# Performance work log

Hardware: AMD Instinct MI355X
Metric: run time of the kernel (lower is better)

## Reference

```python
import jax, jax.numpy as jnp
import numpy as np

B, S, D, H, DH = 2, 2048, 2048, 16, 128
ROT_DIM = 128
ROT_BASE = 10000.0
ATTN_SCALE = float(np.sqrt(DH))


def _sin_cos_rotary(n_ctx, rotary_dim, base):
    pos = jnp.arange(n_ctx, dtype=jnp.float32)
    dim = jnp.arange(rotary_dim // 2, dtype=jnp.float32)
    freq = base ** (dim / (rotary_dim / 2))
    freq = jnp.concatenate([freq, freq])  # non-adjacent pairs: '(2 d)' layout
    angles = pos[:, None] / freq[None, :]  # [n_ctx, rotary_dim]
    return jnp.sin(angles), jnp.cos(angles)


def _rotate_every_two(x):
    # non-adjacent-pairs rotation: [-x2, x1] on halves of last dim
    d = x.shape[-1]
    return jnp.concatenate([-x[..., d // 2:], x[..., :d // 2]], axis=-1)


def _apply_rotary(x, sin, cos):
    # x: [batch, pos, head, d_head]
    n = x.shape[1]
    x_rot = x[..., :ROT_DIM]
    x_pass = x[..., ROT_DIM:]
    c = cos[:n][None, :, None, :]
    s = sin[:n][None, :, None, :]
    x_rotated = x_rot * c + _rotate_every_two(x_rot) * s
    return jnp.concatenate([x_rotated, x_pass], axis=-1)


def setup_inputs() -> dict:
    key = jax.random.key(0)
    ks = jax.random.split(key, 8)
    init = 0.02
    return {
        'query_input': jax.random.normal(ks[0], (B, S, D), jnp.float32),
        'key_input': jax.random.normal(ks[1], (B, S, D), jnp.float32),
        'value_input': jax.random.normal(ks[2], (B, S, D), jnp.float32),
        'W_Q': jax.random.normal(ks[3], (H, D, DH), jnp.float32) * init,
        'W_K': jax.random.normal(ks[4], (H, D, DH), jnp.float32) * init,
        'W_V': jax.random.normal(ks[5], (H, D, DH), jnp.float32) * init,
        'W_O': jax.random.normal(ks[6], (H, DH, D), jnp.float32) * init,
        'b_Q': jnp.zeros((H, DH), jnp.float32),
        'b_K': jnp.zeros((H, DH), jnp.float32),
        'b_V': jnp.zeros((H, DH), jnp.float32),
        'b_O': jnp.zeros((D,), jnp.float32),
    }


def reference(query_input, key_input, value_input, W_Q, W_K, W_V, W_O, b_Q, b_K, b_V, b_O):
    # QKV projections: [b, pos, d_model] x [h, d_model, d_head] -> [b, pos, h, d_head]
    q = jnp.einsum('bpd,hde->bphe', query_input, W_Q) + b_Q
    k = jnp.einsum('bpd,hde->bphe', key_input, W_K) + b_K
    v = jnp.einsum('bpd,hde->bphe', value_input, W_V) + b_V

    sin, cos = _sin_cos_rotary(S, ROT_DIM, ROT_BASE)
    q = _apply_rotary(q, sin, cos)
    k = _apply_rotary(k, sin, cos)

    # attention scores [b, h, q_pos, k_pos]
    scores = jnp.einsum('bqhe,bkhe->bhqk', q, k) / ATTN_SCALE
    causal = jnp.tril(jnp.ones((S, S), bool))
    scores = jnp.where(causal[None, None], scores, -jnp.inf)
    pattern = jax.nn.softmax(scores, axis=-1)
    pattern = jnp.where(jnp.isnan(pattern), jnp.zeros_like(pattern), pattern)

    z = jnp.einsum('bhqk,bkhe->bqhe', pattern, v)
    out = jnp.einsum('bqhe,hed->bqd', z, W_O) + b_O
    return out
```

## Files before the change

kernel.cpp:

```cpp
#include <hip/hip_runtime.h>
#include <hip/hip_bf16.h>
#include <cmath>

typedef __bf16 bf16;
typedef __bf16 bf16x8 __attribute__((ext_vector_type(8)));
typedef __bf16 bf16x4 __attribute__((ext_vector_type(4)));
typedef float  f32x4  __attribute__((ext_vector_type(4)));


__global__ void xcvt_kernel(const float* __restrict__ a, const float* __restrict__ b,
                            const float* __restrict__ c,
                            bf16* __restrict__ oa, bf16* __restrict__ ob, bf16* __restrict__ oc) {
    int i = (blockIdx.x * 256 + threadIdx.x) * 4;
    float4 va = *(const float4*)(a + i);
    float4 vb = *(const float4*)(b + i);
    float4 vc = *(const float4*)(c + i);
    bf16x4 ra = { (bf16)va.x, (bf16)va.y, (bf16)va.z, (bf16)va.w };
    bf16x4 rb = { (bf16)vb.x, (bf16)vb.y, (bf16)vb.z, (bf16)vb.w };
    bf16x4 rc = { (bf16)vc.x, (bf16)vc.y, (bf16)vc.z, (bf16)vc.w };
    *(bf16x4*)(oa + i) = ra;
    *(bf16x4*)(ob + i) = rb;
    *(bf16x4*)(oc + i) = rc;
}

// ... 15 lines not shown
        dst = (z == 0) ? WQT : (z == 1) ? WKT : WVT;
        int h = bx >> 6, rem = bx & 63;
        int d0 = (rem >> 1) << 6, e0 = (rem & 1) << 6;
        sbase = (long)h * 262144 + (long)d0 * 128 + e0;
        sRS = 128;
        dbase = (long)(h * 128 + e0) * 2048 + d0;
    } else {
        src = WO; dst = WOT;
        int a0 = (bx >> 5) << 6, b0 = (bx & 31) << 6;
        sbase = (long)a0 * 2048 + b0;
        sRS = 2048;
        dbase = (long)b0 * 2048 + a0;
    }

#pragma unroll
    for (int p = 0; p < 4; p++) {
        int r = p * 16 + tr;
        float4 v = *(const float4*)(src + sbase + (long)r * sRS + tc);
        T[r * 65 + tc]     = v.x;
        T[r * 65 + tc + 1] = v.y;
        T[r * 65 + tc + 2] = v.z;
        T[r * 65 + tc + 3] = v.w;
    }
    __syncthreads();
#pragma unroll
    for (int p = 0; p < 4; p++) {
        int rr = p * 16 + tr;
        bf16x4 o = { (bf16)T[tc * 65 + rr],       (bf16)T[(tc + 1) * 65 + rr],
                     (bf16)T[(tc + 2) * 65 + rr], (bf16)T[(tc + 3) * 65 + rr] };
        *(bf16x4*)(dst + dbase + (long)rr * 2048 + tc) = o;
    }
}

__launch_bounds__(256)
__global__ void qkv_gemm_kernel(const bf16* __restrict__ XQ, const bf16* __restrict__ XK,
                                const bf16* __restrict__ XV,
                                const bf16* __restrict__ WQT, const bf16* __restrict__ WKT,
                                const bf16* __restrict__ WVT,
                                const float* __restrict__ bQ, const float* __restrict__ bK,
                                const float* __restrict__ bV,
                                bf16* __restrict__ QB, bf16* __restrict__ KB,
                                bf16* __restrict__ VT) {
    __shared__ __align__(16) bf16 As[128 * 32];
    __shared__ __align__(16) bf16 Bs[128 * 32];
    __shared__ __align__(16) bf16 Cs[64 * 136];
    const int z = blockIdx.z;
    const bf16* A  = (z == 0) ? XQ  : (z == 1) ? XK  : XV;
    const bf16* Bm = (z == 0) ? WQT : (z == 1) ? WKT : WVT;
    const float* bias = (z == 0) ? bQ : (z == 1) ? bK : bV;

    const int tid = threadIdx.x;
    const int w = tid >> 6, lane = tid & 63;
    const int quad = lane >> 4, l16 = lane & 15;
    const int wm = w & 1, wn = w >> 1;
    const int m_base = blockIdx.x << 7, n_base = blockIdx.y << 7;

    const int srow = lane >> 2;
    const int scol = (lane & 3) << 3;
    const int ab0 = w * 2, ab1 = w * 2 + 1;
    const bf16* gA0 = A  + (long)(m_base + ab0 * 16 + srow) * 2048 + scol;
    const bf16* gA1 = A  + (long)(m_base + ab1 * 16 + srow) * 2048 + scol;
    const bf16* gB0 = Bm + (long)(n_base + ab0 * 16 + srow) * 2048 + scol;
    const bf16* gB1 = Bm + (long)(n_base + ab1 * 16 + srow) * 2048 + scol;
    bf16* lA0 = &As[ab0 * 512];
    bf16* lA1 = &As[ab1 * 512];
    bf16* lB0 = &Bs[ab0 * 512];
    bf16* lB1 = &Bs[ab1 * 512];

    f32x4 acc[4][4] = {};

    for (int k0 = 0; k0 < 2048; k0 += 32) {
        __builtin_amdgcn_global_load_lds((const __attribute__((address_space(1))) void*)(gA0 + k0),
                                         (__attribute__((address_space(3))) void*)lA0, 16, 0, 0);
        __builtin_amdgcn_global_load_lds((const __attribute__((address_space(1))) void*)(gA1 + k0),
                                         (__attribute__((address_space(3))) void*)lA1, 16, 0, 0);
        __builtin_amdgcn_global_load_lds((const __attribute__((address_space(1))) void*)(gB0 + k0),
                                         (__attribute__((address_space(3))) void*)lB0, 16, 0, 0);
        __builtin_amdgcn_global_load_lds((const __attribute__((address_space(1))) void*)(gB1 + k0),
                                         (__attribute__((address_space(3))) void*)lB1, 16, 0, 0);
        __syncthreads();

        bf16x8 af[4], bfr[4];
#pragma unroll
        for (int mt = 0; mt < 4; mt++)
            af[mt] = *(const bf16x8*)&As[((wm * 64 + mt * 16 + l16) << 5) + (quad << 3)];
#pragma unroll
        for (int nt = 0; nt < 4; nt++) {
            int nrow = wn * 32 + (nt & 1) * 16 + (nt >> 1) * 64 + l16;
            bfr[nt] = *(const bf16x8*)&Bs[(nrow << 5) + (quad << 3)];
        }
#pragma unroll
        for (int mt = 0; mt < 4; mt++)
#pragma unroll
            for (int nt = 0; nt < 4; nt++)
                acc[mt][nt] = __builtin_amdgcn_mfma_f32_16x16x32_bf16(af[mt], bfr[nt], acc[mt][nt], 0, 0, 0);
        __syncthreads();
    }

    const int bq = m_base >> 11;
    const int h  = n_base >> 7;
    const long obase = ((long)(bq * 16 + h)) << 18;

    if (z <= 1) {
        bf16* O = (z == 0) ? QB : KB;
        const float scl = (z == 0) ? 0.08838834764831845f : 1.0f;
#pragma unroll
        for (int nt = 0; nt < 2; nt++) {
            const int e_lo = wn * 32 + nt * 16 + l16;
            const float bv_lo = bias[n_base + e_lo];
            const float bv_hi = bias[n_base + e_lo + 64];
            const float inv_freq = exp2f((float)e_lo * -0.20762050593046f);
#pragma unroll
            for (int mt = 0; mt < 4; mt++) {
#pragma unroll
                for (int r = 0; r < 4; r++) {
                    int s = (m_base & 2047) + wm * 64 + mt * 16 + quad * 4 + r;
                    float sn, cs;
                    __sincosf((float)s * inv_freq, &sn, &cs);
                    float x0 = acc[mt][nt][r]     + bv_lo;
                    float x1 = acc[mt][nt + 2][r] + bv_hi;
                    O[obase + ((long)s << 7) + e_lo]      = (bf16)((x0 * cs - x1 * sn) * scl);
                    O[obase + ((long)s << 7) + e_lo + 64] = (bf16)((x1 * cs + x0 * sn) * scl);
                }
            }
        }
    } else {
#pragma unroll
        for (int eh = 0; eh < 2; eh++) {
#pragma unroll
            for (int nt2 = 0; nt2 < 2; nt2++) {
                const int nt = eh * 2 + nt2;
                const int e_l = wn * 32 + nt2 * 16 + l16;
                const float bv = bias[n_base + eh * 64 + e_l];
#pragma unroll
                for (int mt = 0; mt < 4; mt++) {
                    int s0 = wm * 64 + mt * 16 + quad * 4;
                    bf16x4 pk = { (bf16)(acc[mt][nt][0] + bv), (bf16)(acc[mt][nt][1] + bv),
                                  (bf16)(acc[mt][nt][2] + bv), (bf16)(acc[mt][nt][3] + bv) };
                    *(bf16x4*)&Cs[e_l * 136 + s0] = pk;
                }
            }
            __syncthreads();
            {
                const int e_l = tid >> 2;
                const int sq  = (tid & 3) << 5;
                const int e   = eh * 64 + e_l;
                const long vb = obase + ((long)e << 11) + (m_base & 2047) + sq;
#pragma unroll
                for (int j = 0; j < 4; j++)
                    *(bf16x8*)&VT[vb + j * 8] = *(const bf16x8*)&Cs[e_l * 136 + sq + j * 8];
            }
            __syncthreads();
        }
    }
}

__launch_bounds__(256, 3)
__global__ void flash_kernel(const bf16* __restrict__ Q, const bf16* __restrict__ K,
                             const bf16* __restrict__ Vt, bf16* __restrict__ Z) {
    __shared__ __align__(16) bf16 Ks[64 * 136];
    __shared__ __align__(16) bf16 Vs[128 * 72];
    __shared__ __align__(16) bf16 Ps[64 * 72];
    const int tid = threadIdx.x, w = tid >> 6, lane = tid & 63;
    const int quad = lane >> 4, l16 = lane & 15;
    const int n = blockIdx.x;
    const int bh = (n & 7) | (((n >> 3) & 3) << 3);
    const int qt = 31 - (n >> 5);
    const int b = bh >> 4, h = bh & 15;
    const long qk_base = (long)bh << 18;
    const int qbase = qt << 6;
    const float FM = 12.0f;

    const int kr_row = tid >> 4;
    const int kr_col = (tid & 15) << 3;
    const int vr_row = tid >> 3;
    const int vr_col = (tid & 7) << 3;
    const bf16* Kg = K  + qk_base + (long)kr_row * 128 + kr_col;
    const bf16* Vg = Vt + qk_base + (long)vr_row * 2048 + vr_col;

    bf16x8 qf[4];
#pragma unroll
    for (int ks = 0; ks < 4; ks++)
        qf[ks] = *(const bf16x8*)(Q + qk_base + ((long)(qbase + w * 16 + l16) << 7) + ks * 32 + (quad << 3));

    bf16x8 va[4], ka[4], vb2[4], kb[4];
#pragma unroll
    for (int p = 0; p < 4; p++) va[p] = *(const bf16x8*)(Vg + (long)p * 65536);
// ... 48 lines not shown
                Ps[(w * 16 + quad * 4 + r) * 72 + nt * 16 + l16] = (bf16)p;
            }

#pragma unroll
        for (int kk = 0; kk < 2; kk++) {
            bf16x8 pf = *(const bf16x8*)&Ps[(w * 16 + l16) * 72 + kk * 32 + (quad << 3)];
#pragma unroll
            for (int dt = 0; dt < 8; dt++) {
                bf16x8 vf = *(const bf16x8*)&Vs[(dt * 16 + l16) * 72 + kk * 32 + (quad << 3)];
                o[dt] = __builtin_amdgcn_mfma_f32_16x16x32_bf16(pf, vf, o[dt], 0, 0, 0);
            }
        }
        __syncthreads();

#pragma unroll
        for (int p = 0; p < 4; p++) va[p] = vb2[p];
#pragma unroll
        for (int p = 0; p < 4; p++) ka[p] = kb[p];
    }

#pragma unroll
    for (int r = 0; r < 4; r++) {
        float l = lsum[r];
        l += __shfl_xor(l, 1);
        l += __shfl_xor(l, 2);
        l += __shfl_xor(l, 4);
        l += __shfl_xor(l, 8);
        float inv = 1.f / l;
        int qrow = qbase + w * 16 + quad * 4 + r;
        long zr = ((long)(b * 2048 + qrow) << 11) + h * 128;
#pragma unroll
        for (int dt = 0; dt < 8; dt++)
            Z[zr + dt * 16 + l16] = (bf16)(o[dt][r] * inv);
    }
}

__launch_bounds__(256)
__global__ void gemm_o_kernel(const bf16* __restrict__ A, const bf16* __restrict__ Bm,
                              const float* __restrict__ bias, float* __restrict__ Of) {
    __shared__ __align__(16) bf16 As[128 * 32];
    __shared__ __align__(16) bf16 Bs[128 * 32];
    const int tid = threadIdx.x;
    const int w = tid >> 6, lane = tid & 63;
    const int quad = lane >> 4, l16 = lane & 15;
    const int wm = w & 1, wn = w >> 1;
    const int m_base = blockIdx.x << 7, n_base = blockIdx.y << 7;

    const int srow = lane >> 2;
    const int scol = (lane & 3) << 3;
    const int ab0 = w * 2, ab1 = w * 2 + 1;
    const bf16* gA0 = A  + (long)(m_base + ab0 * 16 + srow) * 2048 + scol;
    const bf16* gA1 = A  + (long)(m_base + ab1 * 16 + srow) * 2048 + scol;
    const bf16* gB0 = Bm + (long)(n_base + ab0 * 16 + srow) * 2048 + scol;
    const bf16* gB1 = Bm + (long)(n_base + ab1 * 16 + srow) * 2048 + scol;
    bf16* lA0 = &As[ab0 * 512];
    bf16* lA1 = &As[ab1 * 512];
    bf16* lB0 = &Bs[ab0 * 512];
    bf16* lB1 = &Bs[ab1 * 512];

    f32x4 acc[4][4] = {};

    for (int k0 = 0; k0 < 2048; k0 += 32) {
        __builtin_amdgcn_global_load_lds((const __attribute__((address_space(1))) void*)(gA0 + k0),
                                         (__attribute__((address_space(3))) void*)lA0, 16, 0, 0);
        __builtin_amdgcn_global_load_lds((const __attribute__((address_space(1))) void*)(gA1 + k0),
                                         (__attribute__((address_space(3))) void*)lA1, 16, 0, 0);
        __builtin_amdgcn_global_load_lds((const __attribute__((address_space(1))) void*)(gB0 + k0),
                                         (__attribute__((address_space(3))) void*)lB0, 16, 0, 0);
        __builtin_amdgcn_global_load_lds((const __attribute__((address_space(1))) void*)(gB1 + k0),
                                         (__attribute__((address_space(3))) void*)lB1, 16, 0, 0);
        __syncthreads();

        bf16x8 af[4], bfr[4];
#pragma unroll
        for (int mt = 0; mt < 4; mt++)
            af[mt] = *(const bf16x8*)&As[((wm * 64 + mt * 16 + l16) << 5) + (quad << 3)];
#pragma unroll
        for (int nt = 0; nt < 4; nt++)
            bfr[nt] = *(const bf16x8*)&Bs[((wn * 64 + nt * 16 + l16) << 5) + (quad << 3)];
#pragma unroll
        for (int mt = 0; mt < 4; mt++)
#pragma unroll
            for (int nt = 0; nt < 4; nt++)
                acc[mt][nt] = __builtin_amdgcn_mfma_f32_16x16x32_bf16(af[mt], bfr[nt], acc[mt][nt], 0, 0, 0);
        __syncthreads();
    }

#pragma unroll
    for (int nt = 0; nt < 4; nt++) {
        int col = n_base + wn * 64 + nt * 16 + l16;
        float bv = bias[col];
#pragma unroll
        for (int mt = 0; mt < 4; mt++) {
#pragma unroll
            for (int r = 0; r < 4; r++) {
                int row = m_base + wm * 64 + mt * 16 + quad * 4 + r;
                Of[((long)row << 11) + col] = acc[mt][nt][r] + bv;
            }
        }
    }
}

extern "C" void kernel_launch(void* const* d_in, const int* in_sizes, int n_in,
                              void* d_out, int out_size, void* d_ws, size_t ws_size,
                              hipStream_t stream) {
    (void)in_sizes; (void)n_in; (void)out_size; (void)ws_size;
    const float* qin = (const float*)d_in[0];
    const float* kin = (const float*)d_in[1];
    const float* vin = (const float*)d_in[2];
    const float* WQ  = (const float*)d_in[3];
    const float* WK  = (const float*)d_in[4];
    const float* WV  = (const float*)d_in[5];
    const float* WO  = (const float*)d_in[6];
    const float* bQ  = (const float*)d_in[7];
    const float* bK  = (const float*)d_in[8];
    const float* bV  = (const float*)d_in[9];
    const float* bO  = (const float*)d_in[10];
    float* out = (float*)d_out;

    bf16* ws = (bf16*)d_ws;
    bf16* XQ  = ws + 0L;
    bf16* XK  = ws + 8388608L;
    bf16* XV  = ws + 16777216L;
    bf16* WQT = ws + 25165824L;
    bf16* WKT = ws + 29360128L;
    bf16* WVT = ws + 33554432L;
    bf16* WOT = ws + 37748736L;
    bf16* QB  = ws + 41943040L;
    bf16* KB  = ws + 50331648L;
    bf16* VT  = ws + 58720256L;
    bf16* Z   = XQ;

    xcvt_kernel<<<8192, 256, 0, stream>>>(qin, kin, vin, XQ, XK, XV);
    wtr_kernel<<<dim3(1024, 4), 256, 0, stream>>>(WQ, WK, WV, WO, WQT, WKT, WVT, WOT);
    qkv_gemm_kernel<<<dim3(32, 16, 3), 256, 0, stream>>>(XQ, XK, XV, WQT, WKT, WVT,
                                                         bQ, bK, bV, QB, KB, VT);
    flash_kernel<<<1024, 256, 0, stream>>>(QB, KB, VT, Z);
    gemm_o_kernel<<<dim3(32, 16), 256, 0, stream>>>(Z, WOT, bO, out);
}
```

Baseline: 426.4 us.

## Rewrite QKV GEMM as 256x256 tile with 8 waves and double-buffered swizzled LDS

The QKV projection GEMM moves from 128x128 tiles with 4 waves to 256x256 tiles with 8 waves (512 threads) and a K-step of 64. Operand tiles are double-buffered in 128 KB of LDS with an XOR swizzle, and global-to-LDS loads for the next stages are interleaved between four MFMA phases using barriers and s_setprio. The goal is more data reuse per byte loaded, fewer LDS bank conflicts, and overlap of memory traffic with matrix math. In exchange the grid shrinks to 384 blocks, occupancy is limited by the large LDS footprint, and the epilogue is reworked to fit the new tile mapping.

```diff
diff --git a/kernel.cpp b/kernel.cpp
--- a/kernel.cpp
+++ b/kernel.cpp
@@ -71,7 +71,7 @@
     }
 }
 
-__launch_bounds__(256)
+__launch_bounds__(512, 2)
 __global__ void qkv_gemm_kernel(const bf16* __restrict__ XQ, const bf16* __restrict__ XK,
                                 const bf16* __restrict__ XV,
                                 const bf16* __restrict__ WQT, const bf16* __restrict__ WKT,
@@ -80,9 +80,7 @@
                                 const float* __restrict__ bV,
                                 bf16* __restrict__ QB, bf16* __restrict__ KB,
                                 bf16* __restrict__ VT) {
-    __shared__ __align__(16) bf16 As[128 * 32];
-    __shared__ __align__(16) bf16 Bs[128 * 32];
-    __shared__ __align__(16) bf16 Cs[64 * 136];
+    __shared__ __align__(1024) char SMb[131072];
     const int z = blockIdx.z;
     const bf16* A  = (z == 0) ? XQ  : (z == 1) ? XK  : XV;
     const bf16* Bm = (z == 0) ? WQT : (z == 1) ? WKT : WVT;
@@ -92,104 +90,178 @@
     const int w = tid >> 6, lane = tid & 63;
     const int quad = lane >> 4, l16 = lane & 15;
     const int wm = w & 1, wn = w >> 1;
-    const int m_base = blockIdx.x << 7, n_base = blockIdx.y << 7;
-
-    const int srow = lane >> 2;
-    const int scol = (lane & 3) << 3;
-    const int ab0 = w * 2, ab1 = w * 2 + 1;
-    const bf16* gA0 = A  + (long)(m_base + ab0 * 16 + srow) * 2048 + scol;
-    const bf16* gA1 = A  + (long)(m_base + ab1 * 16 + srow) * 2048 + scol;
-    const bf16* gB0 = Bm + (long)(n_base + ab0 * 16 + srow) * 2048 + scol;
-    const bf16* gB1 = Bm + (long)(n_base + ab1 * 16 + srow) * 2048 + scol;
-    bf16* lA0 = &As[ab0 * 512];
-    bf16* lA1 = &As[ab1 * 512];
-    bf16* lB0 = &Bs[ab0 * 512];
-    bf16* lB1 = &Bs[ab1 * 512];
-
-    f32x4 acc[4][4] = {};
-
-    for (int k0 = 0; k0 < 2048; k0 += 32) {
-        __builtin_amdgcn_global_load_lds((const __attribute__((address_space(1))) void*)(gA0 + k0),
-                                         (__attribute__((address_space(3))) void*)lA0, 16, 0, 0);
-        __builtin_amdgcn_global_load_lds((const __attribute__((address_space(1))) void*)(gA1 + k0),
-                                         (__attribute__((address_space(3))) void*)lA1, 16, 0, 0);
-        __builtin_amdgcn_global_load_lds((const __attribute__((address_space(1))) void*)(gB0 + k0),
-                                         (__attribute__((address_space(3))) void*)lB0, 16, 0, 0);
-        __builtin_amdgcn_global_load_lds((const __attribute__((address_space(1))) void*)(gB1 + k0),
-                                         (__attribute__((address_space(3))) void*)lB1, 16, 0, 0);
-        __syncthreads();
-
-        bf16x8 af[4], bfr[4];
-#pragma unroll
-        for (int mt = 0; mt < 4; mt++)
-            af[mt] = *(const bf16x8*)&As[((wm * 64 + mt * 16 + l16) << 5) + (quad << 3)];
-#pragma unroll
-        for (int nt = 0; nt < 4; nt++) {
-            int nrow = wn * 32 + (nt & 1) * 16 + (nt >> 1) * 64 + l16;
-            bfr[nt] = *(const bf16x8*)&Bs[(nrow << 5) + (quad << 3)];
-        }
-#pragma unroll
-        for (int mt = 0; mt < 4; mt++)
-#pragma unroll
-            for (int nt = 0; nt < 4; nt++)
-                acc[mt][nt] = __builtin_amdgcn_mfma_f32_16x16x32_bf16(af[mt], bfr[nt], acc[mt][nt], 0, 0, 0);
-        __syncthreads();
-    }
-
-    const int bq = m_base >> 11;
-    const int h  = n_base >> 7;
-    const long obase = ((long)(bq * 16 + h)) << 18;
+    const int m_base = blockIdx.x << 8, n_base = blockIdx.y << 8;
+
+    const int lr = lane >> 3;
+    const int lc = ((lane & 7) ^ lr) << 3;
+    const bf16* gA = A  + (long)(m_base + (w << 4) + lr) * 2048 + lc;
+    const bf16* gB = Bm + (long)(n_base + (w << 4) + lr) * 2048 + lc;
+    char* dstBase = SMb + (w << 11);
+
+#define STAGE(T, opB, half) do {                                                              \
+    const bf16* _s = ((opB) ? gB : gA) + (long)((half) * 128) * 2048 + (T) * 64;              \
+    char* _d = dstBase + (((T) & 1) * 65536 + (opB) * 32768 + (half) * 16384);                \
+    __builtin_amdgcn_global_load_lds((const __attribute__((address_space(1))) void*)_s,       \
+        (__attribute__((address_space(3))) void*)_d, 16, 0, 0);                               \
+    __builtin_amdgcn_global_load_lds((const __attribute__((address_space(1))) void*)(_s + 16384), \
+        (__attribute__((address_space(3))) void*)(_d + 1024), 16, 0, 0);                      \
+} while (0)
+
+    f32x4 acc[8][4] = {};
+    bf16x8 af[4][2], bg[4][2];
+    const int cb0 = quad << 4;
+
+    STAGE(0, 1, 0); STAGE(0, 1, 1); STAGE(0, 0, 0); STAGE(0, 0, 1);
+    STAGE(1, 1, 0); STAGE(1, 1, 1);
+    asm volatile("s_waitcnt vmcnt(4)" ::: "memory");
+    __builtin_amdgcn_s_barrier();
+
+    for (int t = 0; t < 32; ++t) {
+        const int bufA = (t & 1) * 65536 + wm * 16384;
+        const int bufB = (t & 1) * 65536 + 32768 + (wn >> 1) * 16384;
+
+#pragma unroll
+        for (int mt = 0; mt < 4; mt++) {
+            int r = mt * 16 + l16, sw = (r & 7) << 4;
+            af[mt][0] = *(const bf16x8*)(SMb + bufA + r * 128 + (cb0 ^ sw));
+            af[mt][1] = *(const bf16x8*)(SMb + bufA + r * 128 + ((64 + cb0) ^ sw));
+        }
+#pragma unroll
+        for (int nt = 0; nt < 2; nt++) {
+            int r = nt * 64 + (wn & 1) * 32 + l16, sw = (r & 7) << 4;
+            bg[nt][0] = *(const bf16x8*)(SMb + bufB + r * 128 + (cb0 ^ sw));
+            bg[nt][1] = *(const bf16x8*)(SMb + bufB + r * 128 + ((64 + cb0) ^ sw));
+        }
+        if (t < 31) STAGE(t + 1, 0, 0);
+        __builtin_amdgcn_s_barrier();
+        __builtin_amdgcn_s_setprio(1);
+#pragma unroll
+        for (int mt = 0; mt < 4; mt++)
+#pragma unroll
+            for (int nt = 0; nt < 2; nt++) {
+                acc[mt][nt] = __builtin_amdgcn_mfma_f32_16x16x32_bf16(af[mt][0], bg[nt][0], acc[mt][nt], 0, 0, 0);
+                acc[mt][nt] = __builtin_amdgcn_mfma_f32_16x16x32_bf16(af[mt][1], bg[nt][1], acc[mt][nt], 0, 0, 0);
+            }
+        __builtin_amdgcn_s_setprio(0);
+        __builtin_amdgcn_s_barrier();
+
+#pragma unroll
+        for (int nt = 2; nt < 4; nt++) {
+            int r = (nt & 1) * 64 + (wn & 1) * 32 + 16 + l16, sw = (r & 7) << 4;
+            bg[nt][0] = *(const bf16x8*)(SMb + bufB + r * 128 + (cb0 ^ sw));
+            bg[nt][1] = *(const bf16x8*)(SMb + bufB + r * 128 + ((64 + cb0) ^ sw));
+        }
+        if (t < 31) STAGE(t + 1, 0, 1);
+        __builtin_amdgcn_s_barrier();
+        __builtin_amdgcn_s_setprio(1);
+#pragma unroll
+        for (int mt = 0; mt < 4; mt++)
+#pragma unroll
+            for (int nt = 2; nt < 4; nt++) {
+                acc[mt][nt] = __builtin_amdgcn_mfma_f32_16x16x32_bf16(af[mt][0], bg[nt][0], acc[mt][nt], 0, 0, 0);
+                acc[mt][nt] = __builtin_amdgcn_mfma_f32_16x16x32_bf16(af[mt][1], bg[nt][1], acc[mt][nt], 0, 0, 0);
+            }
+        __builtin_amdgcn_s_setprio(0);
+        __builtin_amdgcn_s_barrier();
+
+#pragma unroll
+        for (int mt = 0; mt < 4; mt++) {
+            int r = 64 + mt * 16 + l16, sw = (r & 7) << 4;
+            af[mt][0] = *(const bf16x8*)(SMb + bufA + r * 128 + (cb0 ^ sw));
+            af[mt][1] = *(const bf16x8*)(SMb + bufA + r * 128 + ((64 + cb0) ^ sw));
+        }
+        if (t < 30) STAGE(t + 2, 1, 0);
+        __builtin_amdgcn_s_barrier();
+        __builtin_amdgcn_s_setprio(1);
+#pragma unroll
+        for (int mt = 0; mt < 4; mt++)
+#pragma unroll
+            for (int nt = 2; nt < 4; nt++) {
+                acc[4 + mt][nt] = __builtin_amdgcn_mfma_f32_16x16x32_bf16(af[mt][0], bg[nt][0], acc[4 + mt][nt], 0, 0, 0);
+                acc[4 + mt][nt] = __builtin_amdgcn_mfma_f32_16x16x32_bf16(af[mt][1], bg[nt][1], acc[4 + mt][nt], 0, 0, 0);
+            }
+        __builtin_amdgcn_s_setprio(0);
+        __builtin_amdgcn_s_barrier();
+
+        if (t < 30) STAGE(t + 2, 1, 1);
+        __builtin_amdgcn_s_barrier();
+        __builtin_amdgcn_s_setprio(1);
+#pragma unroll
+        for (int mt = 0; mt < 4; mt++)
+#pragma unroll
+            for (int nt = 0; nt < 2; nt++) {
+                acc[4 + mt][nt] = __builtin_amdgcn_mfma_f32_16x16x32_bf16(af[mt][0], bg[nt][0], acc[4 + mt][nt], 0, 0, 0);
+                acc[4 + mt][nt] = __builtin_amdgcn_mfma_f32_16x16x32_bf16(af[mt][1], bg[nt][1], acc[4 + mt][nt], 0, 0, 0);
+            }
+        __builtin_amdgcn_s_setprio(0);
+        if (t == 30) { asm volatile("s_waitcnt vmcnt(0)" ::: "memory"); }
+        else         { asm volatile("s_waitcnt vmcnt(4)" ::: "memory"); }
+        __builtin_amdgcn_s_barrier();
+    }
+#undef STAGE
+
+    const int bq = blockIdx.x >> 3;
+    const int by = blockIdx.y;
 
     if (z <= 1) {
         bf16* O = (z == 0) ? QB : KB;
         const float scl = (z == 0) ? 0.08838834764831845f : 1.0f;
-#pragma unroll
-        for (int nt = 0; nt < 2; nt++) {
-            const int e_lo = wn * 32 + nt * 16 + l16;
-            const float bv_lo = bias[n_base + e_lo];
-            const float bv_hi = bias[n_base + e_lo + 64];
+        const int h = by * 2 + (wn >> 1);
+        const long obase = ((long)(bq * 16 + h)) << 18;
+#pragma unroll
+        for (int p = 0; p < 2; p++) {
+            const int e_lo = (wn & 1) * 32 + p * 16 + l16;
+            const float bv_lo = bias[n_base + (wn >> 1) * 128 + e_lo];
+            const float bv_hi = bias[n_base + (wn >> 1) * 128 + e_lo + 64];
             const float inv_freq = exp2f((float)e_lo * -0.20762050593046f);
-#pragma unroll
-            for (int mt = 0; mt < 4; mt++) {
+            const int ntL = p * 2, ntH = p * 2 + 1;
+#pragma unroll
+            for (int mt = 0; mt < 8; mt++) {
 #pragma unroll
                 for (int r = 0; r < 4; r++) {
-                    int s = (m_base & 2047) + wm * 64 + mt * 16 + quad * 4 + r;
+                    int s = (m_base & 2047) + wm * 128 + mt * 16 + quad * 4 + r;
                     float sn, cs;
                     __sincosf((float)s * inv_freq, &sn, &cs);
-                    float x0 = acc[mt][nt][r]     + bv_lo;
-                    float x1 = acc[mt][nt + 2][r] + bv_hi;
+                    float x0 = acc[mt][ntL][r] + bv_lo;
+                    float x1 = acc[mt][ntH][r] + bv_hi;
                     O[obase + ((long)s << 7) + e_lo]      = (bf16)((x0 * cs - x1 * sn) * scl);
                     O[obase + ((long)s << 7) + e_lo + 64] = (bf16)((x1 * cs + x0 * sn) * scl);
                 }
             }
         }
     } else {
+        bf16* Ct = (bf16*)SMb;
 #pragma unroll
         for (int eh = 0; eh < 2; eh++) {
-#pragma unroll
-            for (int nt2 = 0; nt2 < 2; nt2++) {
-                const int nt = eh * 2 + nt2;
-                const int e_l = wn * 32 + nt2 * 16 + l16;
-                const float bv = bias[n_base + eh * 64 + e_l];
-#pragma unroll
-                for (int mt = 0; mt < 4; mt++) {
-                    int s0 = wm * 64 + mt * 16 + quad * 4;
-                    bf16x4 pk = { (bf16)(acc[mt][nt][0] + bv), (bf16)(acc[mt][nt][1] + bv),
-                                  (bf16)(acc[mt][nt][2] + bv), (bf16)(acc[mt][nt][3] + bv) };
-                    *(bf16x4*)&Cs[e_l * 136 + s0] = pk;
-                }
+            __syncthreads();
+            if ((wn >> 1) == eh) {
+#pragma unroll
+                for (int p = 0; p < 2; p++)
+#pragma unroll
+                    for (int hi = 0; hi < 2; hi++) {
+                        const int nt = p * 2 + hi;
+                        const int e_l = (wn & 1) * 32 + p * 16 + l16 + hi * 64;
+                        const float bv = bias[n_base + eh * 128 + e_l];
+#pragma unroll
+                        for (int mt = 0; mt < 8; mt++) {
+                            int s0 = wm * 128 + mt * 16 + quad * 4;
+                            bf16x4 pk = { (bf16)(acc[mt][nt][0] + bv), (bf16)(acc[mt][nt][1] + bv),
+                                          (bf16)(acc[mt][nt][2] + bv), (bf16)(acc[mt][nt][3] + bv) };
+                            *(bf16x4*)&Ct[e_l * 264 + s0] = pk;
+                        }
+                    }
             }
             __syncthreads();
             {
                 const int e_l = tid >> 2;
-                const int sq  = (tid & 3) << 5;
-                const int e   = eh * 64 + e_l;
-                const long vb = obase + ((long)e << 11) + (m_base & 2047) + sq;
-#pragma unroll
-                for (int j = 0; j < 4; j++)
-                    *(bf16x8*)&VT[vb + j * 8] = *(const bf16x8*)&Cs[e_l * 136 + sq + j * 8];
-            }
-            __syncthreads();
+                const int sq  = (tid & 3) << 6;
+                const int hgl = by * 2 + eh;
+                const long vb = (((long)(bq * 16 + hgl)) << 18) + ((long)e_l << 11)
+                              + (m_base & 2047) + sq;
+#pragma unroll
+                for (int j = 0; j < 8; j++)
+                    *(bf16x8*)&VT[vb + j * 8] = *(const bf16x8*)&Ct[e_l * 264 + sq + j * 8];
+            }
         }
     }
 }
@@ -407,8 +479,8 @@
 
     xcvt_kernel<<<8192, 256, 0, stream>>>(qin, kin, vin, XQ, XK, XV);
     wtr_kernel<<<dim3(1024, 4), 256, 0, stream>>>(WQ, WK, WV, WO, WQT, WKT, WVT, WOT);
-    qkv_gemm_kernel<<<dim3(32, 16, 3), 256, 0, stream>>>(XQ, XK, XV, WQT, WKT, WVT,
-                                                         bQ, bK, bV, QB, KB, VT);
+    qkv_gemm_kernel<<<dim3(16, 8, 3), 512, 0, stream>>>(XQ, XK, XV, WQT, WKT, WVT,
+                                                        bQ, bK, bV, QB, KB, VT);
     flash_kernel<<<1024, 256, 0, stream>>>(QB, KB, VT, Z);
     gemm_o_kernel<<<dim3(32, 16), 256, 0, stream>>>(Z, WOT, bO, out);
 }
```

After: 437.8 us. +2.7%, slower.

## Rewrite QKV GEMM with 256x128 tiles, 512 threads, double-buffered swizzled LDS

Applied to the files above, without the earlier changes.

The QKV projection GEMM now uses 512-thread blocks computing 256x128 tiles with BK=64. Global-to-LDS loads are double-buffered across iterations and overlapped with MFMA work using explicit waitcnt, barriers and setprio. An XOR swizzle on the LDS layout avoids bank conflicts. The aim is to hide load latency and raise MFMA utilisation, at the cost of 96KB of LDS per block, which limits occupancy, and of fewer blocks in the grid.

```diff
diff --git a/kernel.cpp b/kernel.cpp
--- a/kernel.cpp
+++ b/kernel.cpp
@@ -71,7 +71,7 @@
     }
 }
 
-__launch_bounds__(256)
+__launch_bounds__(512, 2)
 __global__ void qkv_gemm_kernel(const bf16* __restrict__ XQ, const bf16* __restrict__ XK,
                                 const bf16* __restrict__ XV,
                                 const bf16* __restrict__ WQT, const bf16* __restrict__ WKT,
@@ -80,9 +80,7 @@
                                 const float* __restrict__ bV,
                                 bf16* __restrict__ QB, bf16* __restrict__ KB,
                                 bf16* __restrict__ VT) {
-    __shared__ __align__(16) bf16 As[128 * 32];
-    __shared__ __align__(16) bf16 Bs[128 * 32];
-    __shared__ __align__(16) bf16 Cs[64 * 136];
+    __shared__ __align__(1024) char SMb[98304];
     const int z = blockIdx.z;
     const bf16* A  = (z == 0) ? XQ  : (z == 1) ? XK  : XV;
     const bf16* Bm = (z == 0) ? WQT : (z == 1) ? WKT : WVT;
@@ -92,104 +90,131 @@
     const int w = tid >> 6, lane = tid & 63;
     const int quad = lane >> 4, l16 = lane & 15;
     const int wm = w & 1, wn = w >> 1;
-    const int m_base = blockIdx.x << 7, n_base = blockIdx.y << 7;
-
-    const int srow = lane >> 2;
-    const int scol = (lane & 3) << 3;
-    const int ab0 = w * 2, ab1 = w * 2 + 1;
-    const bf16* gA0 = A  + (long)(m_base + ab0 * 16 + srow) * 2048 + scol;
-    const bf16* gA1 = A  + (long)(m_base + ab1 * 16 + srow) * 2048 + scol;
-    const bf16* gB0 = Bm + (long)(n_base + ab0 * 16 + srow) * 2048 + scol;
-    const bf16* gB1 = Bm + (long)(n_base + ab1 * 16 + srow) * 2048 + scol;
-    bf16* lA0 = &As[ab0 * 512];
-    bf16* lA1 = &As[ab1 * 512];
-    bf16* lB0 = &Bs[ab0 * 512];
-    bf16* lB1 = &Bs[ab1 * 512];
-
-    f32x4 acc[4][4] = {};
-
-    for (int k0 = 0; k0 < 2048; k0 += 32) {
-        __builtin_amdgcn_global_load_lds((const __attribute__((address_space(1))) void*)(gA0 + k0),
-                                         (__attribute__((address_space(3))) void*)lA0, 16, 0, 0);
-        __builtin_amdgcn_global_load_lds((const __attribute__((address_space(1))) void*)(gA1 + k0),
-                                         (__attribute__((address_space(3))) void*)lA1, 16, 0, 0);
-        __builtin_amdgcn_global_load_lds((const __attribute__((address_space(1))) void*)(gB0 + k0),
-                                         (__attribute__((address_space(3))) void*)lB0, 16, 0, 0);
-        __builtin_amdgcn_global_load_lds((const __attribute__((address_space(1))) void*)(gB1 + k0),
-                                         (__attribute__((address_space(3))) void*)lB1, 16, 0, 0);
-        __syncthreads();
-
-        bf16x8 af[4], bfr[4];
-#pragma unroll
-        for (int mt = 0; mt < 4; mt++)
-            af[mt] = *(const bf16x8*)&As[((wm * 64 + mt * 16 + l16) << 5) + (quad << 3)];
-#pragma unroll
-        for (int nt = 0; nt < 4; nt++) {
-            int nrow = wn * 32 + (nt & 1) * 16 + (nt >> 1) * 64 + l16;
-            bfr[nt] = *(const bf16x8*)&Bs[(nrow << 5) + (quad << 3)];
-        }
-#pragma unroll
-        for (int mt = 0; mt < 4; mt++)
-#pragma unroll
-            for (int nt = 0; nt < 4; nt++)
-                acc[mt][nt] = __builtin_amdgcn_mfma_f32_16x16x32_bf16(af[mt], bfr[nt], acc[mt][nt], 0, 0, 0);
-        __syncthreads();
-    }
-
-    const int bq = m_base >> 11;
-    const int h  = n_base >> 7;
+    const int m_base = blockIdx.x << 8;
+    const int h = blockIdx.y;
+    const int n_base = h << 7;
+
+    const int lr = lane >> 3;
+    const int lc = ((lane & 7) ^ lr) << 3;
+    const bf16* gA = A  + (long)(m_base + (w << 4) + lr) * 2048 + lc;
+    const bf16* gB = Bm + (long)(n_base + (w << 4) + lr) * 2048 + lc;
+
+#define STAGE_A(T, half) do {                                                                 \
+    const bf16* _s = gA + (long)((half) * 128) * 2048 + (T) * 64;                             \
+    char* _d = SMb + ((T) & 1) * 32768 + (half) * 16384 + (w << 11);                          \
+    __builtin_amdgcn_global_load_lds((const __attribute__((address_space(1))) void*)_s,       \
+        (__attribute__((address_space(3))) void*)_d, 16, 0, 0);                               \
+    __builtin_amdgcn_global_load_lds((const __attribute__((address_space(1))) void*)(_s + 16384), \
+        (__attribute__((address_space(3))) void*)(_d + 1024), 16, 0, 0);                      \
+} while (0)
+#define STAGE_B(T) do {                                                                       \
+    const bf16* _s = gB + (T) * 64;                                                           \
+    char* _d = SMb + 65536 + ((T) & 1) * 16384 + (w << 11);                                   \
+    __builtin_amdgcn_global_load_lds((const __attribute__((address_space(1))) void*)_s,       \
+        (__attribute__((address_space(3))) void*)_d, 16, 0, 0);                               \
+    __builtin_amdgcn_global_load_lds((const __attribute__((address_space(1))) void*)(_s + 16384), \
+        (__attribute__((address_space(3))) void*)(_d + 1024), 16, 0, 0);                      \
+} while (0)
+#define RD(buf, row, kh) \
+    (*(const bf16x8*)(SMb + (buf) + (row) * 128 + ((((kh) * 64) + cb0) ^ (((row) & 7) << 4))))
+
+    f32x4 acc[8][2] = {};
+    bf16x8 af[8], bg[2];
+    const int cb0 = quad << 4;
+    const int rB0 = wn * 16 + l16;
+
+    STAGE_B(0); STAGE_A(0, 0); STAGE_A(0, 1); STAGE_B(1);
+    asm volatile("s_waitcnt vmcnt(2)" ::: "memory");
+    __builtin_amdgcn_s_barrier();
+
+    for (int t = 0; t < 32; ++t) {
+        const int bufA = (t & 1) * 32768 + wm * 16384;
+        const int bufB = 65536 + (t & 1) * 16384;
+
+#pragma unroll
+        for (int mt = 0; mt < 8; mt++) af[mt] = RD(bufA, mt * 16 + l16, 0);
+        bg[0] = RD(bufB, rB0, 0);
+        bg[1] = RD(bufB, rB0 + 64, 0);
+        if (t < 31) STAGE_A(t + 1, 0);
+        __builtin_amdgcn_s_barrier();
+        __builtin_amdgcn_s_setprio(1);
+#pragma unroll
+        for (int mt = 0; mt < 8; mt++) {
+            acc[mt][0] = __builtin_amdgcn_mfma_f32_16x16x32_bf16(af[mt], bg[0], acc[mt][0], 0, 0, 0);
+            acc[mt][1] = __builtin_amdgcn_mfma_f32_16x16x32_bf16(af[mt], bg[1], acc[mt][1], 0, 0, 0);
+        }
+        __builtin_amdgcn_s_setprio(0);
+        __builtin_amdgcn_s_barrier();
+
+#pragma unroll
+        for (int mt = 0; mt < 8; mt++) af[mt] = RD(bufA, mt * 16 + l16, 1);
+        bg[0] = RD(bufB, rB0, 1);
+        bg[1] = RD(bufB, rB0 + 64, 1);
+        if (t < 31) STAGE_A(t + 1, 1);
+        asm volatile("s_waitcnt lgkmcnt(0)" ::: "memory");
+        __builtin_amdgcn_sched_barrier(0);
+        __builtin_amdgcn_s_barrier();
+        if (t < 30) STAGE_B(t + 2);
+        __builtin_amdgcn_s_setprio(1);
+#pragma unroll
+        for (int mt = 0; mt < 8; mt++) {
+            acc[mt][0] = __builtin_amdgcn_mfma_f32_16x16x32_bf16(af[mt], bg[0], acc[mt][0], 0, 0, 0);
+            acc[mt][1] = __builtin_amdgcn_mfma_f32_16x16x32_bf16(af[mt], bg[1], acc[mt][1], 0, 0, 0);
+        }
+        __builtin_amdgcn_s_setprio(0);
+        if (t == 30) { asm volatile("s_waitcnt vmcnt(0)" ::: "memory"); }
+        else         { asm volatile("s_waitcnt vmcnt(2)" ::: "memory"); }
+        __builtin_amdgcn_s_barrier();
+    }
+#undef STAGE_A
+#undef STAGE_B
+#undef RD
+
+    const int bq = blockIdx.x >> 3;
     const long obase = ((long)(bq * 16 + h)) << 18;
 
     if (z <= 1) {
         bf16* O = (z == 0) ? QB : KB;
         const float scl = (z == 0) ? 0.08838834764831845f : 1.0f;
+        const int e_lo = wn * 16 + l16;
+        const float bv_lo = bias[n_base + e_lo];
+        const float bv_hi = bias[n_base + e_lo + 64];
+        const float inv_freq = exp2f((float)e_lo * -0.20762050593046f);
+#pragma unroll
+        for (int mt = 0; mt < 8; mt++) {
+#pragma unroll
+            for (int r = 0; r < 4; r++) {
+                int s = (m_base & 2047) + wm * 128 + mt * 16 + quad * 4 + r;
+                float sn, cs;
+                __sincosf((float)s * inv_freq, &sn, &cs);
+                float x0 = acc[mt][0][r] + bv_lo;
+                float x1 = acc[mt][1][r] + bv_hi;
+                O[obase + ((long)s << 7) + e_lo]      = (bf16)((x0 * cs - x1 * sn) * scl);
+                O[obase + ((long)s << 7) + e_lo + 64] = (bf16)((x1 * cs + x0 * sn) * scl);
+            }
+        }
+    } else {
+        bf16* Ct = (bf16*)SMb;
 #pragma unroll
         for (int nt = 0; nt < 2; nt++) {
-            const int e_lo = wn * 32 + nt * 16 + l16;
-            const float bv_lo = bias[n_base + e_lo];
-            const float bv_hi = bias[n_base + e_lo + 64];
-            const float inv_freq = exp2f((float)e_lo * -0.20762050593046f);
-#pragma unroll
-            for (int mt = 0; mt < 4; mt++) {
-#pragma unroll
-                for (int r = 0; r < 4; r++) {
-                    int s = (m_base & 2047) + wm * 64 + mt * 16 + quad * 4 + r;
-                    float sn, cs;
-                    __sincosf((float)s * inv_freq, &sn, &cs);
-                    float x0 = acc[mt][nt][r]     + bv_lo;
-                    float x1 = acc[mt][nt + 2][r] + bv_hi;
-                    O[obase + ((long)s << 7) + e_lo]      = (bf16)((x0 * cs - x1 * sn) * scl);
-                    O[obase + ((long)s << 7) + e_lo + 64] = (bf16)((x1 * cs + x0 * sn) * scl);
-                }
-            }
-        }
-    } else {
-#pragma unroll
-        for (int eh = 0; eh < 2; eh++) {
-#pragma unroll
-            for (int nt2 = 0; nt2 < 2; nt2++) {
-                const int nt = eh * 2 + nt2;
-                const int e_l = wn * 32 + nt2 * 16 + l16;
-                const float bv = bias[n_base + eh * 64 + e_l];
-#pragma unroll
-                for (int mt = 0; mt < 4; mt++) {
-                    int s0 = wm * 64 + mt * 16 + quad * 4;
-                    bf16x4 pk = { (bf16)(acc[mt][nt][0] + bv), (bf16)(acc[mt][nt][1] + bv),
-                                  (bf16)(acc[mt][nt][2] + bv), (bf16)(acc[mt][nt][3] + bv) };
-                    *(bf16x4*)&Cs[e_l * 136 + s0] = pk;
-                }
-            }
-            __syncthreads();
-            {
-                const int e_l = tid >> 2;
-                const int sq  = (tid & 3) << 5;
-                const int e   = eh * 64 + e_l;
-                const long vb = obase + ((long)e << 11) + (m_base & 2047) + sq;
-#pragma unroll
-                for (int j = 0; j < 4; j++)
-                    *(bf16x8*)&VT[vb + j * 8] = *(const bf16x8*)&Cs[e_l * 136 + sq + j * 8];
-            }
-            __syncthreads();
+            const int e_l = nt * 64 + wn * 16 + l16;
+            const float bv = bias[n_base + e_l];
+#pragma unroll
+            for (int mt = 0; mt < 8; mt++) {
+                int s0 = wm * 128 + mt * 16 + quad * 4;
+                bf16x4 pk = { (bf16)(acc[mt][nt][0] + bv), (bf16)(acc[mt][nt][1] + bv),
+                              (bf16)(acc[mt][nt][2] + bv), (bf16)(acc[mt][nt][3] + bv) };
+                *(bf16x4*)&Ct[e_l * 264 + s0] = pk;
+            }
+        }
+        __syncthreads();
+        {
+            const int e_l = tid >> 2;
+            const int sq  = (tid & 3) << 6;
+            const long vb = obase + ((long)e_l << 11) + (m_base & 2047) + sq;
+#pragma unroll
+            for (int j = 0; j < 8; j++)
+                *(bf16x8*)&VT[vb + j * 8] = *(const bf16x8*)&Ct[e_l * 264 + sq + j * 8];
         }
     }
 }
@@ -407,7 +432,7 @@
 
     xcvt_kernel<<<8192, 256, 0, stream>>>(qin, kin, vin, XQ, XK, XV);
     wtr_kernel<<<dim3(1024, 4), 256, 0, stream>>>(WQ, WK, WV, WO, WQT, WKT, WVT, WOT);
-    qkv_gemm_kernel<<<dim3(32, 16, 3), 256, 0, stream>>>(XQ, XK, XV, WQT, WKT, WVT,
+    qkv_gemm_kernel<<<dim3(16, 16, 3), 512, 0, stream>>>(XQ, XK, XV, WQT, WKT, WVT,
                                                          bQ, bK, bV, QB, KB, VT);
     flash_kernel<<<1024, 256, 0, stream>>>(QB, KB, VT, Z);
     gemm_o_kernel<<<dim3(32, 16), 256, 0, stream>>>(Z, WOT, bO, out);
```

Result: no change. 428.3 us (+0.4%).

## Use triple-buffered swizzled 256x128 ring GEMM for QKV and output projections

Applied to the files above, without the earlier changes.

Both projection GEMMs now share one macro-based main loop. It runs 512-thread blocks on a 256x128 output tile with a 64-wide k step. Tiles are staged into a three-slot LDS ring using async global-to-LDS loads two steps ahead, so there is only one barrier per iteration, with XOR swizzling to avoid bank conflicts and raised wave priority around the MFMA block. The aim is to hide global load latency and cut barrier and LDS overhead compared with the old single-buffered 128x128, k=32 loop. In exchange it uses about 144KB of LDS per block, which limits occupancy to one block per CU, and it halves the grid size.

```diff
diff --git a/kernel.cpp b/kernel.cpp
--- a/kernel.cpp
+++ b/kernel.cpp
@@ -71,7 +71,73 @@
     }
 }
 
-__launch_bounds__(256)
+
+#define GLOAD(S, D) __builtin_amdgcn_global_load_lds( \
+    (const __attribute__((address_space(1))) void*)(S), \
+    (__attribute__((address_space(3))) void*)(D), 16, 0, 0)
+
+#define STAGE_T(T, slotOff) do {                                     \
+    const bf16* _sa = gA + (long)(T) * 64;                           \
+    char* _da = SMb + (slotOff) + (w << 12);                         \
+    GLOAD(_sa,         _da);                                         \
+    GLOAD(_sa + 16384, _da + 1024);                                  \
+    GLOAD(_sa + 32768, _da + 2048);                                  \
+    GLOAD(_sa + 49152, _da + 3072);                                  \
+    const bf16* _sb = gB + (long)(T) * 64;                           \
+    char* _db = SMb + (slotOff) + 32768 + (w << 11);                 \
+    GLOAD(_sb,         _db);                                         \
+    GLOAD(_sb + 16384, _db + 1024);                                  \
+} while (0)
+
+#define RD_A(r, kh) (*(const bf16x8*)(SMb + curS + (r) * 128 + ((((kh) << 6) + cb0) ^ sw)))
+#define RD_B(r, kh) (*(const bf16x8*)(SMb + curS + 32768 + (r) * 128 + ((((kh) << 6) + cb0) ^ sw)))
+
+#define RING_GEMM_LOOP                                                                 \
+    f32x4 acc[4][4] = {};                                                              \
+    const int cb0 = quad << 4;                                                         \
+    const int sw  = (l16 & 7) << 4;                                                    \
+    STAGE_T(0, 0);                                                                     \
+    STAGE_T(1, 49152);                                                                 \
+    asm volatile("s_waitcnt vmcnt(6)" ::: "memory");                                   \
+    int curS = 0, stgS = 98304;                                                        \
+    _Pragma("unroll 1")                                                                \
+    for (int t = 0; t < 32; ++t) {                                                     \
+        __builtin_amdgcn_s_barrier();                                                  \
+        __builtin_amdgcn_sched_barrier(0);                                             \
+        if (t < 30) STAGE_T(t + 2, stgS);                                              \
+        bf16x8 bgf[2][2][2];                                                           \
+        _Pragma("unroll")                                                              \
+        for (int hi = 0; hi < 2; hi++)                                                 \
+            _Pragma("unroll")                                                          \
+            for (int nt2 = 0; nt2 < 2; nt2++) {                                        \
+                int rB = wn * 32 + nt2 * 16 + hi * 64 + l16;                           \
+                bgf[hi][nt2][0] = RD_B(rB, 0);                                         \
+                bgf[hi][nt2][1] = RD_B(rB, 1);                                         \
+            }                                                                          \
+        __builtin_amdgcn_s_setprio(1);                                                 \
+        _Pragma("unroll")                                                              \
+        for (int mt = 0; mt < 4; mt++) {                                               \
+            int rA = wm * 64 + mt * 16 + l16;                                          \
+            bf16x8 a0 = RD_A(rA, 0);                                                   \
+            bf16x8 a1 = RD_A(rA, 1);                                                   \
+            _Pragma("unroll")                                                          \
+            for (int hi = 0; hi < 2; hi++)                                             \
+                _Pragma("unroll")                                                      \
+                for (int nt2 = 0; nt2 < 2; nt2++) {                                    \
+                    acc[mt][hi * 2 + nt2] = __builtin_amdgcn_mfma_f32_16x16x32_bf16(   \
+                        a0, bgf[hi][nt2][0], acc[mt][hi * 2 + nt2], 0, 0, 0);          \
+                    acc[mt][hi * 2 + nt2] = __builtin_amdgcn_mfma_f32_16x16x32_bf16(   \
+                        a1, bgf[hi][nt2][1], acc[mt][hi * 2 + nt2], 0, 0, 0);          \
+                }                                                                      \
+        }                                                                              \
+        __builtin_amdgcn_s_setprio(0);                                                 \
+        if (t == 30) { asm volatile("s_waitcnt vmcnt(0)" ::: "memory"); }              \
+        else         { asm volatile("s_waitcnt vmcnt(6)" ::: "memory"); }              \
+        curS = (curS == 98304) ? 0 : curS + 49152;                                     \
+        stgS = (stgS == 98304) ? 0 : stgS + 49152;                                     \
+    }
+
+__launch_bounds__(512, 2)
 __global__ void qkv_gemm_kernel(const bf16* __restrict__ XQ, const bf16* __restrict__ XK,
                                 const bf16* __restrict__ XV,
                                 const bf16* __restrict__ WQT, const bf16* __restrict__ WKT,
@@ -80,9 +146,7 @@
                                 const float* __restrict__ bV,
                                 bf16* __restrict__ QB, bf16* __restrict__ KB,
                                 bf16* __restrict__ VT) {
-    __shared__ __align__(16) bf16 As[128 * 32];
-    __shared__ __align__(16) bf16 Bs[128 * 32];
-    __shared__ __align__(16) bf16 Cs[64 * 136];
+    __shared__ __align__(1024) char SMb[147456];
     const int z = blockIdx.z;
     const bf16* A  = (z == 0) ? XQ  : (z == 1) ? XK  : XV;
     const bf16* Bm = (z == 0) ? WQT : (z == 1) ? WKT : WVT;
@@ -91,61 +155,26 @@
     const int tid = threadIdx.x;
     const int w = tid >> 6, lane = tid & 63;
     const int quad = lane >> 4, l16 = lane & 15;
-    const int wm = w & 1, wn = w >> 1;
-    const int m_base = blockIdx.x << 7, n_base = blockIdx.y << 7;
-
-    const int srow = lane >> 2;
-    const int scol = (lane & 3) << 3;
-    const int ab0 = w * 2, ab1 = w * 2 + 1;
-    const bf16* gA0 = A  + (long)(m_base + ab0 * 16 + srow) * 2048 + scol;
-    const bf16* gA1 = A  + (long)(m_base + ab1 * 16 + srow) * 2048 + scol;
-    const bf16* gB0 = Bm + (long)(n_base + ab0 * 16 + srow) * 2048 + scol;
-    const bf16* gB1 = Bm + (long)(n_base + ab1 * 16 + srow) * 2048 + scol;
-    bf16* lA0 = &As[ab0 * 512];
-    bf16* lA1 = &As[ab1 * 512];
-    bf16* lB0 = &Bs[ab0 * 512];
-    bf16* lB1 = &Bs[ab1 * 512];
-
-    f32x4 acc[4][4] = {};
-
-    for (int k0 = 0; k0 < 2048; k0 += 32) {
-        __builtin_amdgcn_global_load_lds((const __attribute__((address_space(1))) void*)(gA0 + k0),
-                                         (__attribute__((address_space(3))) void*)lA0, 16, 0, 0);
-        __builtin_amdgcn_global_load_lds((const __attribute__((address_space(1))) void*)(gA1 + k0),
-                                         (__attribute__((address_space(3))) void*)lA1, 16, 0, 0);
-        __builtin_amdgcn_global_load_lds((const __attribute__((address_space(1))) void*)(gB0 + k0),
-                                         (__attribute__((address_space(3))) void*)lB0, 16, 0, 0);
-        __builtin_amdgcn_global_load_lds((const __attribute__((address_space(1))) void*)(gB1 + k0),
-                                         (__attribute__((address_space(3))) void*)lB1, 16, 0, 0);
-        __syncthreads();
-
-        bf16x8 af[4], bfr[4];
-#pragma unroll
-        for (int mt = 0; mt < 4; mt++)
-            af[mt] = *(const bf16x8*)&As[((wm * 64 + mt * 16 + l16) << 5) + (quad << 3)];
-#pragma unroll
-        for (int nt = 0; nt < 4; nt++) {
-            int nrow = wn * 32 + (nt & 1) * 16 + (nt >> 1) * 64 + l16;
-            bfr[nt] = *(const bf16x8*)&Bs[(nrow << 5) + (quad << 3)];
-        }
-#pragma unroll
-        for (int mt = 0; mt < 4; mt++)
-#pragma unroll
-            for (int nt = 0; nt < 4; nt++)
-                acc[mt][nt] = __builtin_amdgcn_mfma_f32_16x16x32_bf16(af[mt], bfr[nt], acc[mt][nt], 0, 0, 0);
-        __syncthreads();
-    }
-
-    const int bq = m_base >> 11;
-    const int h  = n_base >> 7;
-    const long obase = ((long)(bq * 16 + h)) << 18;
+    const int wm = w >> 1, wn = w & 1;
+    const int m_base = blockIdx.x << 8;
+    const int n_base = blockIdx.y << 7;
+
+    const int lr = lane >> 3;
+    const int lc = ((lane & 7) ^ lr) << 3;
+    const bf16* gA = A  + (long)(m_base + (w << 5) + lr) * 2048 + lc;
+    const bf16* gB = Bm + (long)(n_base + (w << 4) + lr) * 2048 + lc;
+
+    RING_GEMM_LOOP
+
+    const int bq = blockIdx.x >> 3;
+    const long obase = ((long)(bq * 16 + blockIdx.y)) << 18;
 
     if (z <= 1) {
         bf16* O = (z == 0) ? QB : KB;
         const float scl = (z == 0) ? 0.08838834764831845f : 1.0f;
 #pragma unroll
-        for (int nt = 0; nt < 2; nt++) {
-            const int e_lo = wn * 32 + nt * 16 + l16;
+        for (int nt2 = 0; nt2 < 2; nt2++) {
+            const int e_lo = wn * 32 + nt2 * 16 + l16;
             const float bv_lo = bias[n_base + e_lo];
             const float bv_hi = bias[n_base + e_lo + 64];
             const float inv_freq = exp2f((float)e_lo * -0.20762050593046f);
@@ -156,42 +185,77 @@
                     int s = (m_base & 2047) + wm * 64 + mt * 16 + quad * 4 + r;
                     float sn, cs;
                     __sincosf((float)s * inv_freq, &sn, &cs);
-                    float x0 = acc[mt][nt][r]     + bv_lo;
-                    float x1 = acc[mt][nt + 2][r] + bv_hi;
+                    float x0 = acc[mt][nt2][r]     + bv_lo;
+                    float x1 = acc[mt][2 + nt2][r] + bv_hi;
                     O[obase + ((long)s << 7) + e_lo]      = (bf16)((x0 * cs - x1 * sn) * scl);
                     O[obase + ((long)s << 7) + e_lo + 64] = (bf16)((x1 * cs + x0 * sn) * scl);
                 }
             }
         }
     } else {
-#pragma unroll
-        for (int eh = 0; eh < 2; eh++) {
+        __syncthreads();
+        bf16* Ct = (bf16*)SMb;
+#pragma unroll
+        for (int hi = 0; hi < 2; hi++)
 #pragma unroll
             for (int nt2 = 0; nt2 < 2; nt2++) {
-                const int nt = eh * 2 + nt2;
-                const int e_l = wn * 32 + nt2 * 16 + l16;
-                const float bv = bias[n_base + eh * 64 + e_l];
+                const int e_l = wn * 32 + nt2 * 16 + hi * 64 + l16;
+                const float bv = bias[n_base + e_l];
 #pragma unroll
                 for (int mt = 0; mt < 4; mt++) {
                     int s0 = wm * 64 + mt * 16 + quad * 4;
-                    bf16x4 pk = { (bf16)(acc[mt][nt][0] + bv), (bf16)(acc[mt][nt][1] + bv),
-                                  (bf16)(acc[mt][nt][2] + bv), (bf16)(acc[mt][nt][3] + bv) };
-                    *(bf16x4*)&Cs[e_l * 136 + s0] = pk;
+                    bf16x4 pk = { (bf16)(acc[mt][hi * 2 + nt2][0] + bv),
+                                  (bf16)(acc[mt][hi * 2 + nt2][1] + bv),
+                                  (bf16)(acc[mt][hi * 2 + nt2][2] + bv),
+                                  (bf16)(acc[mt][hi * 2 + nt2][3] + bv) };
+                    *(bf16x4*)&Ct[e_l * 264 + s0] = pk;
                 }
             }
-            __syncthreads();
-            {
-                const int e_l = tid >> 2;
-                const int sq  = (tid & 3) << 5;
-                const int e   = eh * 64 + e_l;
-                const long vb = obase + ((long)e << 11) + (m_base & 2047) + sq;
-#pragma unroll
-                for (int j = 0; j < 4; j++)
-                    *(bf16x8*)&VT[vb + j * 8] = *(const bf16x8*)&Cs[e_l * 136 + sq + j * 8];
-            }
-            __syncthreads();
-        }
-    }
+        __syncthreads();
+        {
+            const int e_l = tid >> 2;
+            const int sq  = (tid & 3) << 6;
+            const long vb = obase + ((long)e_l << 11) + (m_base & 2047) + sq;
+#pragma unroll
+            for (int j = 0; j < 8; j++)
+                *(bf16x8*)&VT[vb + j * 8] = *(const bf16x8*)&Ct[e_l * 264 + sq + j * 8];
+        }
+    }
+}
+
+__launch_bounds__(512, 2)
+__global__ void gemm_o_kernel(const bf16* __restrict__ A, const bf16* __restrict__ Bm,
+                              const float* __restrict__ bias, float* __restrict__ Of) {
+    __shared__ __align__(1024) char SMb[147456];
+    const int tid = threadIdx.x;
+    const int w = tid >> 6, lane = tid & 63;
+    const int quad = lane >> 4, l16 = lane & 15;
+    const int wm = w >> 1, wn = w & 1;
+    const int m_base = blockIdx.x << 8;
+    const int n_base = blockIdx.y << 7;
+
+    const int lr = lane >> 3;
+    const int lc = ((lane & 7) ^ lr) << 3;
+    const bf16* gA = A  + (long)(m_base + (w << 5) + lr) * 2048 + lc;
+    const bf16* gB = Bm + (long)(n_base + (w << 4) + lr) * 2048 + lc;
+
+    RING_GEMM_LOOP
+
+#pragma unroll
+    for (int hi = 0; hi < 2; hi++)
+#pragma unroll
+        for (int nt2 = 0; nt2 < 2; nt2++) {
+            int col = n_base + wn * 32 + nt2 * 16 + hi * 64 + l16;
+            float bv = bias[col];
+#pragma unroll
+            for (int mt = 0; mt < 4; mt++) {
+#pragma unroll
+                for (int r = 0; r < 4; r++) {
+                    int row = m_base + wm * 64 + mt * 16 + quad * 4 + r;
+                    Of[((long)row << 11) + col] = acc[mt][hi * 2 + nt2][r] + bv;
+                }
+            }
+        }
 }
 
 __launch_bounds__(256, 3)
@@ -306,72 +370,6 @@
 #pragma unroll
         for (int dt = 0; dt < 8; dt++)
             Z[zr + dt * 16 + l16] = (bf16)(o[dt][r] * inv);
-    }
-}
-
-__launch_bounds__(256)
-__global__ void gemm_o_kernel(const bf16* __restrict__ A, const bf16* __restrict__ Bm,
-                              const float* __restrict__ bias, float* __restrict__ Of) {
-    __shared__ __align__(16) bf16 As[128 * 32];
-    __shared__ __align__(16) bf16 Bs[128 * 32];
-    const int tid = threadIdx.x;
-    const int w = tid >> 6, lane = tid & 63;
-    const int quad = lane >> 4, l16 = lane & 15;
-    const int wm = w & 1, wn = w >> 1;
-    const int m_base = blockIdx.x << 7, n_base = blockIdx.y << 7;
-
-    const int srow = lane >> 2;
-    const int scol = (lane & 3) << 3;
-    const int ab0 = w * 2, ab1 = w * 2 + 1;
-    const bf16* gA0 = A  + (long)(m_base + ab0 * 16 + srow) * 2048 + scol;
-    const bf16* gA1 = A  + (long)(m_base + ab1 * 16 + srow) * 2048 + scol;
-    const bf16* gB0 = Bm + (long)(n_base + ab0 * 16 + srow) * 2048 + scol;
-    const bf16* gB1 = Bm + (long)(n_base + ab1 * 16 + srow) * 2048 + scol;
-    bf16* lA0 = &As[ab0 * 512];
-    bf16* lA1 = &As[ab1 * 512];
-    bf16* lB0 = &Bs[ab0 * 512];
-    bf16* lB1 = &Bs[ab1 * 512];
-
-    f32x4 acc[4][4] = {};
-
-    for (int k0 = 0; k0 < 2048; k0 += 32) {
-        __builtin_amdgcn_global_load_lds((const __attribute__((address_space(1))) void*)(gA0 + k0),
-                                         (__attribute__((address_space(3))) void*)lA0, 16, 0, 0);
-        __builtin_amdgcn_global_load_lds((const __attribute__((address_space(1))) void*)(gA1 + k0),
-                                         (__attribute__((address_space(3))) void*)lA1, 16, 0, 0);
-        __builtin_amdgcn_global_load_lds((const __attribute__((address_space(1))) void*)(gB0 + k0),
-                                         (__attribute__((address_space(3))) void*)lB0, 16, 0, 0);
-        __builtin_amdgcn_global_load_lds((const __attribute__((address_space(1))) void*)(gB1 + k0),
-                                         (__attribute__((address_space(3))) void*)lB1, 16, 0, 0);
-        __syncthreads();
-
-        bf16x8 af[4], bfr[4];
-#pragma unroll
-        for (int mt = 0; mt < 4; mt++)
-            af[mt] = *(const bf16x8*)&As[((wm * 64 + mt * 16 + l16) << 5) + (quad << 3)];
-#pragma unroll
-        for (int nt = 0; nt < 4; nt++)
-            bfr[nt] = *(const bf16x8*)&Bs[((wn * 64 + nt * 16 + l16) << 5) + (quad << 3)];
-#pragma unroll
-        for (int mt = 0; mt < 4; mt++)
-#pragma unroll
-            for (int nt = 0; nt < 4; nt++)
-                acc[mt][nt] = __builtin_amdgcn_mfma_f32_16x16x32_bf16(af[mt], bfr[nt], acc[mt][nt], 0, 0, 0);
-        __syncthreads();
-    }
-
-#pragma unroll
-    for (int nt = 0; nt < 4; nt++) {
-        int col = n_base + wn * 64 + nt * 16 + l16;
-        float bv = bias[col];
-#pragma unroll
-        for (int mt = 0; mt < 4; mt++) {
-#pragma unroll
-            for (int r = 0; r < 4; r++) {
-                int row = m_base + wm * 64 + mt * 16 + quad * 4 + r;
-                Of[((long)row << 11) + col] = acc[mt][nt][r] + bv;
-            }
-        }
     }
 }
 
@@ -407,8 +405,8 @@
 
     xcvt_kernel<<<8192, 256, 0, stream>>>(qin, kin, vin, XQ, XK, XV);
     wtr_kernel<<<dim3(1024, 4), 256, 0, stream>>>(WQ, WK, WV, WO, WQT, WKT, WVT, WOT);
-    qkv_gemm_kernel<<<dim3(32, 16, 3), 256, 0, stream>>>(XQ, XK, XV, WQT, WKT, WVT,
+    qkv_gemm_kernel<<<dim3(16, 16, 3), 512, 0, stream>>>(XQ, XK, XV, WQT, WKT, WVT,
                                                          bQ, bK, bV, QB, KB, VT);
     flash_kernel<<<1024, 256, 0, stream>>>(QB, KB, VT, Z);
-    gemm_o_kernel<<<dim3(32, 16), 256, 0, stream>>>(Z, WOT, bO, out);
-}
+    gemm_o_kernel<<<dim3(16, 16), 512, 0, stream>>>(Z, WOT, bO, out);
+}
```

After: 409.6 us. 1.04x faster.
